# Performance work log

Hardware: AMD Instinct MI355X
Metric: run time of the kernel (lower is better)

## Reference

```python
import jax, jax.numpy as jnp
import numpy as np

N = 50000        # nodes
E = 600000       # edges
D = 128          # hidden dim
FID = 128        # fixed_input_dim (one-hot size)
RWSE = 16        # rwse_dim
G = 128          # num graphs
L = 4            # num GIN blocks
DEG = 1001       # degree embedding table (clamp to 1000)
GIN_EPS = 0.0
BN_EPS = 1e-5


def setup_inputs() -> dict:
    key = jax.random.key(0)
    ks = jax.random.split(key, 16)
    s = 0.05
    inp = {
        "feat_id": jax.random.randint(ks[0], (N,), 0, 100000),
        "edge_index": jax.random.randint(ks[1], (2, E), 0, N),
        "batch_idx": jnp.sort(jax.random.randint(ks[2], (N,), 0, G)),
        "rwse": jax.random.normal(ks[3], (N, RWSE), jnp.float32),
        "in_degrees": jax.random.randint(ks[4], (N,), 0, DEG),
        # parameters
        "value_W": jax.random.normal(ks[5], (FID, D), jnp.float32) * s,
        "value_b": jnp.zeros((D,), jnp.float32),
        "rwse_W": jax.random.normal(ks[6], (RWSE, D), jnp.float32) * s,
        "rwse_b": jnp.zeros((D,), jnp.float32),
        "deg_emb": jax.random.normal(ks[7], (DEG, D), jnp.float32) * s,
        "mlp_W1": jax.random.normal(ks[8], (L, D, D), jnp.float32) * s,
        "mlp_b1": jnp.zeros((L, D), jnp.float32),
        "mlp_W2": jax.random.normal(ks[9], (L, D, D), jnp.float32) * s,
        "mlp_b2": jnp.zeros((L, D), jnp.float32),
        "bn_gamma": 1.0 + jax.random.normal(ks[10], (L, D), jnp.float32) * s,
        "bn_beta": jax.random.normal(ks[11], (L, D), jnp.float32) * s,
        "bn_mean": jax.random.normal(ks[12], (L, D), jnp.float32) * s,
        "bn_var": 1.0 + jax.random.uniform(ks[13], (L, D), jnp.float32) * 0.1,
    }
    return inp


def reference(feat_id, edge_index, batch_idx, rwse, in_degrees,
              value_W, value_b, rwse_W, rwse_b, deg_emb,
              mlp_W1, mlp_b1, mlp_W2, mlp_b2,
              bn_gamma, bn_beta, bn_mean, bn_var):
    # one_hot(feat_id % FID) @ value_W  ==  row gather of value_W
    h_id = jnp.remainder(feat_id, FID)
    h_attr = value_W[h_id] + value_b                      # [N, D]
    h_attr = h_attr + rwse @ rwse_W + rwse_b              # rwse projection
    deg = jnp.clip(in_degrees, 0, DEG - 1)
    h = h_attr + deg_emb[deg]                             # [N, D]

    src, dst = edge_index[0], edge_index[1]
    for l in range(L):
        # GIN aggregation: sum of neighbor messages + (1+eps)*self
        agg = jax.ops.segment_sum(h[src], dst, num_segments=N)
        agg = agg + (1.0 + GIN_EPS) * h
        # MLP: Linear -> ReLU -> Linear
        m = jax.nn.relu(agg @ mlp_W1[l] + mlp_b1[l]) @ mlp_W2[l] + mlp_b2[l]
        # BatchNorm (inference stats) + ReLU
        inv = bn_gamma[l] * jax.lax.rsqrt(bn_var[l] + BN_EPS)
        h = jax.nn.relu((m - bn_mean[l]) * inv + bn_beta[l])

    # scatter-mean graph pooling
    pooled = jax.ops.segment_sum(h, batch_idx, num_segments=G)      # [G, D]
    count = jax.ops.segment_sum(jnp.ones((N, 1), h.dtype), batch_idx,
                                num_segments=G)                     # [G, 1]
    graph_feature = pooled / jnp.maximum(count, 1.0)
    return graph_feature, h
```

## Files before the change

### kernel.cpp

```cpp
#include <hip/hip_runtime.h>

#define N_NODES 50000
#define N_EDGES 600000
#define DIM 128
#define NGRAPH 128
#define NLAYER 4
#define BN_EPS 1e-5f
#define SCAN_BLK 1024
#define MROWS 64

#define EN_BLOCKS 3125
#define WT_BLOCKS 512
#define HB_BLOCKS 2344

using short8  = __attribute__((ext_vector_type(8))) short;
using float4v = __attribute__((ext_vector_type(4))) float;

__device__ __forceinline__ float bf2f(unsigned short u) {
    union { unsigned int i; float f; } c; c.i = ((unsigned int)u) << 16; return c.f;
}
__device__ __forceinline__ unsigned short f2bf(float f) {
    union { float f; unsigned int i; } c; c.f = f;
    unsigned int x = c.i;
    return (unsigned short)((x + 0x7fffu + ((x >> 16) & 1u)) >> 16);
}

__global__ void fused_pre_kernel(const int* __restrict__ feat_id,
                                 const float* __restrict__ rwse,
                                 const int* __restrict__ indeg,
                                 const float* __restrict__ value_W,
                                 const float* __restrict__ value_b,
                                 const float* __restrict__ rwse_W,
                                 const float* __restrict__ rwse_b,
                                 const float* __restrict__ deg_emb,
                                 unsigned short* __restrict__ hout,
                                 const float* __restrict__ W1,
                                 const float* __restrict__ W2,
                                 unsigned short* __restrict__ w1t,
                                 unsigned short* __restrict__ w2t,
                                 const int* __restrict__ dst,
                                 int* __restrict__ cnt)
{
    int b = blockIdx.x;
    if (b < EN_BLOCKS) {
        __shared__ float srw[16][16];
        __shared__ int   sfid[16], sdeg[16];
        const int t = threadIdx.x;
        const int base = b * 16;
        srw[t >> 4][t & 15] = rwse[(size_t)base * 16 + t];
        if (t < 16) sfid[t] = feat_id[base + t] & 127;
        else if (t < 32) {
            int dg = indeg[base + t - 16];
            sdeg[t - 16] = dg < 0 ? 0 : (dg > 1000 ? 1000 : dg);
        }
        const int d = t & 127, half = t >> 7;
        float wk[16];
#pragma unroll
        for (int k = 0; k < 16; ++k) wk[k] = rwse_W[k * DIM + d];
        float vb = value_b[d] + rwse_b[d];
        __syncthreads();
#pragma unroll
        for (int nn = 0; nn < 8; ++nn) {
            int nl = half * 8 + nn;
            int node = base + nl;
            float v = value_W[sfid[nl] * DIM + d] + vb + deg_emb[sdeg[nl] * DIM + d];
            float acc = 0.f;
#pragma unroll
            for (int k = 0; k < 16; ++k) acc += srw[nl][k] * wk[k];
            hout[(size_t)node * DIM + d] = f2bf(v + acc);
        }
    } else if (b < EN_BLOCKS + WT_BLOCKS) {
        int idx = (b - EN_BLOCKS) * 256 + threadIdx.x;
        int i = idx & (DIM * DIM - 1);
        int l = (idx >> 14) & 3;
        int is2 = idx >= NLAYER * DIM * DIM;
        int n = i >> 7, k = i & 127;
        const float* W = (is2 ? W2 : W1) + l * DIM * DIM;
        unsigned short v = f2bf(W[k * DIM + n]);
        (is2 ? w2t : w1t)[l * DIM * DIM + n * DIM + k] = v;
    } else {
        int e = (b - EN_BLOCKS - WT_BLOCKS) * 256 + threadIdx.x;
        if (e < N_EDGES) atomicAdd(&cnt[dst[e]], 1);
    }
}

__global__ void scanA_kernel(const int* __restrict__ cnt, int* __restrict__ rp, int* __restrict__ bsum) {
    __shared__ int sc[SCAN_BLK];
    int t = threadIdx.x, i = blockIdx.x * SCAN_BLK + t;
    int v = (i < N_NODES) ? cnt[i] : 0;
    sc[t] = v; __syncthreads();
    for (int off = 1; off < SCAN_BLK; off <<= 1) {
        int add = (t >= off) ? sc[t - off] : 0;
        __syncthreads();
        sc[t] += add;
        __syncthreads();
    }
    if (i < N_NODES) rp[i] = sc[t] - v;
    if (t == SCAN_BLK - 1) bsum[blockIdx.x] = sc[t];
}

__global__ void scan_fixup_kernel(int* __restrict__ rp, const int* __restrict__ bsum,
                                  int* __restrict__ cur, int nsb) {
    __shared__ int sbx[64];
    int t = threadIdx.x;
    if (t < 64) {
        int v = (t < nsb) ? bsum[t] : 0;
        int orig = v;
        for (int off = 1; off < 64; off <<= 1) {
            int y = __shfl_up(v, off, 64);
            if (t >= off) v += y;
        }
        sbx[t] = v - orig;
    }
    __syncthreads();
    int i = blockIdx.x * 256 + t;
    if (i < N_NODES) { int v = rp[i] + sbx[i >> 10]; rp[i] = v; cur[i] = v; }
    else if (i == N_NODES) rp[i] = N_EDGES;
}

__global__ void scatter_kernel(const int* __restrict__ src, const int* __restrict__ dst,
                               int* __restrict__ cur, int* __restrict__ esrc) {
    int e = blockIdx.x * blockDim.x + threadIdx.x;
    if (e < N_EDGES) {
        int pos = atomicAdd(&cur[dst[e]], 1);
        esrc[pos] = src[e];
    }
}

__global__ void __launch_bounds__(256) agg_kernel(const unsigned short* __restrict__ hin,
                                                  const int* __restrict__ rp,
                                                  const int* __restrict__ esrc,
                                                  unsigned short* __restrict__ aggout)
{
    int node = (blockIdx.x * blockDim.x + threadIdx.x) >> 6;
    node = __builtin_amdgcn_readfirstlane(node);
    if (node >= N_NODES) return;
    int lane = threadIdx.x & 63;
    int grp = lane >> 4, q = lane & 15;

    float a[8];
    if (grp == 0) {
        uint4 s = *(const uint4*)(hin + (size_t)node * DIM + q * 8);
        a[0] = bf2f((unsigned short)(s.x & 0xffff)); a[1] = bf2f((unsigned short)(s.x >> 16));
        a[2] = bf2f((unsigned short)(s.y & 0xffff)); a[3] = bf2f((unsigned short)(s.y >> 16));
        a[4] = bf2f((unsigned short)(s.z & 0xffff)); a[5] = bf2f((unsigned short)(s.z >> 16));
        a[6] = bf2f((unsigned short)(s.w & 0xffff)); a[7] = bf2f((unsigned short)(s.w >> 16));
    } else {
#pragma unroll
        for (int i = 0; i < 8; ++i) a[i] = 0.f;
    }

    const int e1 = rp[node + 1];
    int e = rp[node] + grp;
    bool p0 = e < e1, p1 = e + 4 < e1;
    int s0 = p0 ? esrc[e] : 0;
    int s1 = p1 ? esrc[e + 4] : 0;
    while (p0) {
        uint4 v0 = *(const uint4*)(hin + (size_t)s0 * DIM + q * 8);
        uint4 v1;
        if (p1) v1 = *(const uint4*)(hin + (size_t)s1 * DIM + q * 8);
        else v1 = (uint4){0u, 0u, 0u, 0u};
        e += 8;
        p0 = e < e1; p1 = e + 4 < e1;
        s0 = p0 ? esrc[e] : 0;
        s1 = p1 ? esrc[e + 4] : 0;
        a[0] += bf2f((unsigned short)(v0.x & 0xffff)) + bf2f((unsigned short)(v1.x & 0xffff));
        a[1] += bf2f((unsigned short)(v0.x >> 16))    + bf2f((unsigned short)(v1.x >> 16));
        a[2] += bf2f((unsigned short)(v0.y & 0xffff)) + bf2f((unsigned short)(v1.y & 0xffff));
        a[3] += bf2f((unsigned short)(v0.y >> 16))    + bf2f((unsigned short)(v1.y >> 16));
        a[4] += bf2f((unsigned short)(v0.z & 0xffff)) + bf2f((unsigned short)(v1.z & 0xffff));
        a[5] += bf2f((unsigned short)(v0.z >> 16))    + bf2f((unsigned short)(v1.z >> 16));
        a[6] += bf2f((unsigned short)(v0.w & 0xffff)) + bf2f((unsigned short)(v1.w & 0xffff));
        a[7] += bf2f((unsigned short)(v0.w >> 16))    + bf2f((unsigned short)(v1.w >> 16));
    }

#pragma unroll
    for (int i = 0; i < 8; ++i) {
        a[i] += __shfl_xor(a[i], 16, 64);
        a[i] += __shfl_xor(a[i], 32, 64);
    }

    if (grp == 0) {
        uint4 o;
        o.x = (unsigned int)f2bf(a[0]) | ((unsigned int)f2bf(a[1]) << 16);
        o.y = (unsigned int)f2bf(a[2]) | ((unsigned int)f2bf(a[3]) << 16);
        o.z = (unsigned int)f2bf(a[4]) | ((unsigned int)f2bf(a[5]) << 16);
        o.w = (unsigned int)f2bf(a[6]) | ((unsigned int)f2bf(a[7]) << 16);
        *(uint4*)(aggout + (size_t)node * DIM + q * 8) = o;
    }
}

__global__ void __launch_bounds__(256, 4) mlp_kernel(
    const unsigned short* __restrict__ aggin,
    const unsigned short* __restrict__ w1t,
    const unsigned short* __restrict__ w2t,
    const float* __restrict__ b1, const float* __restrict__ b2,
    const float* __restrict__ gam, const float* __restrict__ bet,
    const float* __restrict__ mean, const float* __restrict__ var,
    unsigned short* __restrict__ hout, float* __restrict__ fout, int last)
{
    __shared__ unsigned short sM[MROWS * DIM];
    const int tid = threadIdx.x;
    const int wave = tid >> 6, lane = tid & 63;
    const int fr = lane & 15, fg = lane >> 4;
    const int rowbase = blockIdx.x * MROWS;

    int arow = rowbase + wave * 16 + fr;
    if (arow >= N_NODES) arow = N_NODES - 1;
    const unsigned short* aptr = aggin + (size_t)arow * DIM + fg * 8;

    float4v acc[8];
#pragma unroll
    for (int n = 0; n < 8; ++n) acc[n] = (float4v){0.f, 0.f, 0.f, 0.f};

#pragma unroll
    for (int ks = 0; ks < 4; ++ks) {
        short8 a0 = *(const short8*)(aptr + ks * 32);
#pragma unroll
        for (int nb = 0; nb < 8; ++nb) {
            short8 b = *(const short8*)(w1t + (nb * 16 + fr) * DIM + ks * 32 + fg * 8);
            acc[nb] = __builtin_amdgcn_mfma_f32_16x16x32_bf16(a0, b, acc[nb], 0, 0, 0);
        }
    }

#pragma unroll
    for (int nb = 0; nb < 8; ++nb) {
        int col = nb * 16 + fr;
        float bias = b1[col];
#pragma unroll
        for (int r = 0; r < 4; ++r) {
            int row = wave * 16 + fg * 4 + r;
            float v = acc[nb][r] + bias;
            v = fmaxf(v, 0.f);
            int byte = row * 256 + col * 2; byte ^= (row & 7) << 4;
            *(unsigned short*)((char*)sM + byte) = f2bf(v);
        }
    }
    __syncthreads();

    float4v acc2[8];
#pragma unroll
    for (int n = 0; n < 8; ++n) acc2[n] = (float4v){0.f, 0.f, 0.f, 0.f};

#pragma unroll
    for (int ks = 0; ks < 4; ++ks) {
        int k0 = ks * 32 + fg * 8;
        short8 a0;
        { int row = wave * 16 + fr; int byte = row * 256 + k0 * 2; byte ^= (row & 7) << 4; a0 = *(const short8*)((char*)sM + byte); }
#pragma unroll
        for (int nb = 0; nb < 8; ++nb) {
            short8 b = *(const short8*)(w2t + (nb * 16 + fr) * DIM + k0);
            acc2[nb] = __builtin_amdgcn_mfma_f32_16x16x32_bf16(a0, b, acc2[nb], 0, 0, 0);
        }
    }

#pragma unroll
    for (int nb = 0; nb < 8; ++nb) {
        int col = nb * 16 + fr;
        float bias = b2[col];
        float iv = gam[col] * rsqrtf(var[col] + BN_EPS);
        float mn = mean[col], bt = bet[col];
#pragma unroll
        for (int r = 0; r < 4; ++r) {
            int row = wave * 16 + fg * 4 + r;
            int node = rowbase + row;
            if (node < N_NODES) {
                float v = acc2[nb][r] + bias;
                v = (v - mn) * iv + bt;
                v = fmaxf(v, 0.f);
                if (last) fout[(size_t)node * DIM + col] = v;
                else hout[(size_t)node * DIM + col] = f2bf(v);
            }
        }
    }
}

__global__ void __launch_bounds__(256) pool_partial_kernel(const float* __restrict__ h,
                                                           const int* __restrict__ batch,
                                                           float* __restrict__ partial)
{
    __shared__ float sums[256];
    __shared__ int sb[2];
    int g = blockIdx.x >> 3, split = blockIdx.x & 7;
    if (threadIdx.x < 2) {
        int target = g + threadIdx.x;
        int lo = 0, hi = N_NODES;
        while (lo < hi) { int mid = (lo + hi) >> 1; if (batch[mid] < target) lo = mid + 1; else hi = mid; }
        sb[threadIdx.x] = lo;
    }
    __syncthreads();
    int lo = sb[0], hi = sb[1];
    int d = threadIdx.x & 127, half = threadIdx.x >> 7;
    float acc = 0.f;
    for (int n = lo + split * 2 + half; n < hi; n += 16) acc += h[(size_t)n * DIM + d];
    sums[threadIdx.x] = acc;
    __syncthreads();
    if (threadIdx.x < 128)
        partial[blockIdx.x * DIM + threadIdx.x] = sums[threadIdx.x] + sums[threadIdx.x + 128];
}

__global__ void pool_comb_kernel(const float* __restrict__ partial,
                                 const int* __restrict__ batch,
                                 float* __restrict__ out)
{
    __shared__ int sb[2];
    int g = blockIdx.x, t = threadIdx.x;
    if (t < 2) {
        int target = g + t;
        int lo = 0, hi = N_NODES;
        while (lo < hi) { int mid = (lo + hi) >> 1; if (batch[mid] < target) lo = mid + 1; else hi = mid; }
        sb[t] = lo;
    }
    __syncthreads();
    float s = 0.f;
#pragma unroll
    for (int sp = 0; sp < 8; ++sp) s += partial[(g * 8 + sp) * DIM + t];
    float c = (float)(sb[1] - sb[0]);
    out[g * DIM + t] = s / fmaxf(c, 1.f);
}

extern "C" void kernel_launch(void* const* d_in, const int* in_sizes, int n_in,
                              void* d_out, int out_size, void* d_ws, size_t ws_size,
                              hipStream_t stream)
{
    const int*   feat_id = (const int*)d_in[0];
    const int*   eidx    = (const int*)d_in[1];
    const int*   batch   = (const int*)d_in[2];
    const float* rwse    = (const float*)d_in[3];
    const int*   indeg   = (const int*)d_in[4];
    const float* value_W = (const float*)d_in[5];
    const float* value_b = (const float*)d_in[6];
    const float* rwse_W  = (const float*)d_in[7];
    const float* rwse_b  = (const float*)d_in[8];
    const float* deg_emb = (const float*)d_in[9];
    const float* W1      = (const float*)d_in[10];
    const float* b1      = (const float*)d_in[11];
    const float* W2      = (const float*)d_in[12];
    const float* b2      = (const float*)d_in[13];
    const float* gam     = (const float*)d_in[14];
    const float* bet     = (const float*)d_in[15];
    const float* mean    = (const float*)d_in[16];
    const float* var     = (const float*)d_in[17];

    const int* srcv = eidx;
    const int* dstv = eidx + N_EDGES;

    char* p = (char*)d_ws;
    auto alloc = [&](size_t bytes) { char* r = p; p += (bytes + 255) & ~(size_t)255; return r; };
    unsigned short* hA   = (unsigned short*)alloc((size_t)N_NODES * DIM * 2);
    unsigned short* agg  = (unsigned short*)alloc((size_t)N_NODES * DIM * 2);
    int* cnt  = (int*)alloc((size_t)N_NODES * 4);
    int* rp   = (int*)alloc((size_t)(N_NODES + 1) * 4);
    int* cur  = (int*)alloc((size_t)N_NODES * 4);
    int* bsum = (int*)alloc(64 * 4);
    int* esrc = (int*)alloc((size_t)N_EDGES * 4);
    unsigned short* w1t = (unsigned short*)alloc((size_t)NLAYER * DIM * DIM * 2);
    unsigned short* w2t = (unsigned short*)alloc((size_t)NLAYER * DIM * DIM * 2);
    float* partial = (float*)alloc((size_t)NGRAPH * 8 * DIM * 4);

    float* out = (float*)d_out;
    float* hf  = out + NGRAPH * DIM;

    hipMemsetAsync(cnt, 0, (size_t)N_NODES * 4, stream);
    fused_pre_kernel<<<EN_BLOCKS + WT_BLOCKS + HB_BLOCKS, 256, 0, stream>>>(
        feat_id, rwse, indeg, value_W, value_b, rwse_W, rwse_b, deg_emb, hA,
        W1, W2, w1t, w2t, dstv, cnt);
    int nsb = (N_NODES + SCAN_BLK - 1) / SCAN_BLK;
    scanA_kernel<<<nsb, SCAN_BLK, 0, stream>>>(cnt, rp, bsum);
    scan_fixup_kernel<<<(N_NODES + 1 + 255) / 256, 256, 0, stream>>>(rp, bsum, cur, nsb);
    scatter_kernel<<<(N_EDGES + 255) / 256, 256, 0, stream>>>(srcv, dstv, cur, esrc);

    const int nrb = (N_NODES + MROWS - 1) / MROWS;
    for (int l = 0; l < NLAYER; ++l) {
        agg_kernel<<<(N_NODES * 64 + 255) / 256, 256, 0, stream>>>(hA, rp, esrc, agg);
        mlp_kernel<<<nrb, 256, 0, stream>>>(agg,
            w1t + l * DIM * DIM, w2t + l * DIM * DIM,
            b1 + l * DIM, b2 + l * DIM, gam + l * DIM, bet + l * DIM,
            mean + l * DIM, var + l * DIM,
            hA, hf, (l == NLAYER - 1) ? 1 : 0);
    }
    pool_partial_kernel<<<NGRAPH * 8, 256, 0, stream>>>(hf, batch, partial);
    pool_comb_kernel<<<NGRAPH, DIM, 0, stream>>>(partial, batch, out);
}
```

Baseline: 455.0 us.

## Shrink MLP blocks to one wave per 16 rows and simplify neighbor gather loop

The MLP kernel now runs one 64-thread wave per 16-row tile instead of four waves per 64 rows. It hoists all four A-operand k-slices into registers and loads the four B slices per output block together before issuing the MFMAs. Because 50000 divides by 16, the tail-row bounds checks are removed. The aggregation loop drops the two-edge unrolled gather in favor of one edge per iteration with the next source index prefetched, which reduces memory-level parallelism per lane. The smaller blocks give more scheduling granularity but shrink weight reuse across waves within a block.

```diff
diff --git a/kernel.cpp b/kernel.cpp
--- a/kernel.cpp
+++ b/kernel.cpp
@@ -7,7 +7,6 @@
 #define NLAYER 4
 #define BN_EPS 1e-5f
 #define SCAN_BLK 1024
-#define MROWS 64
 
 #define EN_BLOCKS 3125
 #define WT_BLOCKS 512
@@ -150,28 +149,19 @@
         for (int i = 0; i < 8; ++i) a[i] = 0.f;
     }
 
-    const int e1 = rp[node + 1];
+    int e1 = rp[node + 1];
     int e = rp[node] + grp;
-    bool p0 = e < e1, p1 = e + 4 < e1;
-    int s0 = p0 ? esrc[e] : 0;
-    int s1 = p1 ? esrc[e + 4] : 0;
-    while (p0) {
-        uint4 v0 = *(const uint4*)(hin + (size_t)s0 * DIM + q * 8);
-        uint4 v1;
-        if (p1) v1 = *(const uint4*)(hin + (size_t)s1 * DIM + q * 8);
-        else v1 = (uint4){0u, 0u, 0u, 0u};
-        e += 8;
-        p0 = e < e1; p1 = e + 4 < e1;
-        s0 = p0 ? esrc[e] : 0;
-        s1 = p1 ? esrc[e + 4] : 0;
-        a[0] += bf2f((unsigned short)(v0.x & 0xffff)) + bf2f((unsigned short)(v1.x & 0xffff));
-        a[1] += bf2f((unsigned short)(v0.x >> 16))    + bf2f((unsigned short)(v1.x >> 16));
-        a[2] += bf2f((unsigned short)(v0.y & 0xffff)) + bf2f((unsigned short)(v1.y & 0xffff));
-        a[3] += bf2f((unsigned short)(v0.y >> 16))    + bf2f((unsigned short)(v1.y >> 16));
-        a[4] += bf2f((unsigned short)(v0.z & 0xffff)) + bf2f((unsigned short)(v1.z & 0xffff));
-        a[5] += bf2f((unsigned short)(v0.z >> 16))    + bf2f((unsigned short)(v1.z >> 16));
-        a[6] += bf2f((unsigned short)(v0.w & 0xffff)) + bf2f((unsigned short)(v1.w & 0xffff));
-        a[7] += bf2f((unsigned short)(v0.w >> 16))    + bf2f((unsigned short)(v1.w >> 16));
+    int snext = (e < e1) ? esrc[e] : 0;
+    while (e < e1) {
+        int s = snext;
+        int en = e + 4;
+        snext = (en < e1) ? esrc[en] : 0;
+        uint4 v = *(const uint4*)(hin + (size_t)s * DIM + q * 8);
+        a[0] += bf2f((unsigned short)(v.x & 0xffff)); a[1] += bf2f((unsigned short)(v.x >> 16));
+        a[2] += bf2f((unsigned short)(v.y & 0xffff)); a[3] += bf2f((unsigned short)(v.y >> 16));
+        a[4] += bf2f((unsigned short)(v.z & 0xffff)); a[5] += bf2f((unsigned short)(v.z >> 16));
+        a[6] += bf2f((unsigned short)(v.w & 0xffff)); a[7] += bf2f((unsigned short)(v.w >> 16));
+        e = en;
     }
 
 #pragma unroll
@@ -190,7 +180,7 @@
     }
 }
 
-__global__ void __launch_bounds__(256, 4) mlp_kernel(
+__global__ void __launch_bounds__(64, 4) mlp_kernel(
     const unsigned short* __restrict__ aggin,
     const unsigned short* __restrict__ w1t,
     const unsigned short* __restrict__ w2t,
@@ -199,28 +189,33 @@
     const float* __restrict__ mean, const float* __restrict__ var,
     unsigned short* __restrict__ hout, float* __restrict__ fout, int last)
 {
-    __shared__ unsigned short sM[MROWS * DIM];
-    const int tid = threadIdx.x;
-    const int wave = tid >> 6, lane = tid & 63;
+    __shared__ unsigned short sM[16 * DIM];
+    const int lane = threadIdx.x;
     const int fr = lane & 15, fg = lane >> 4;
-    const int rowbase = blockIdx.x * MROWS;
-
-    int arow = rowbase + wave * 16 + fr;
-    if (arow >= N_NODES) arow = N_NODES - 1;
-    const unsigned short* aptr = aggin + (size_t)arow * DIM + fg * 8;
+    const int rowbase = blockIdx.x * 16;
+
+    const unsigned short* aptr = aggin + (size_t)(rowbase + fr) * DIM + fg * 8;
+    short8 a0 = *(const short8*)(aptr);
+    short8 a1 = *(const short8*)(aptr + 32);
+    short8 a2 = *(const short8*)(aptr + 64);
+    short8 a3 = *(const short8*)(aptr + 96);
 
     float4v acc[8];
 #pragma unroll
     for (int n = 0; n < 8; ++n) acc[n] = (float4v){0.f, 0.f, 0.f, 0.f};
 
-#pragma unroll
-    for (int ks = 0; ks < 4; ++ks) {
-        short8 a0 = *(const short8*)(aptr + ks * 32);
-#pragma unroll
-        for (int nb = 0; nb < 8; ++nb) {
-            short8 b = *(const short8*)(w1t + (nb * 16 + fr) * DIM + ks * 32 + fg * 8);
-            acc[nb] = __builtin_amdgcn_mfma_f32_16x16x32_bf16(a0, b, acc[nb], 0, 0, 0);
-        }
+    const unsigned short* bp1 = w1t + fr * DIM + fg * 8;
+#pragma unroll
+    for (int nb = 0; nb < 8; ++nb) {
+        const unsigned short* bb = bp1 + nb * 16 * DIM;
+        short8 b0 = *(const short8*)(bb);
+        short8 b1v = *(const short8*)(bb + 32);
+        short8 b2v = *(const short8*)(bb + 64);
+        short8 b3v = *(const short8*)(bb + 96);
+        acc[nb] = __builtin_amdgcn_mfma_f32_16x16x32_bf16(a0, b0, acc[nb], 0, 0, 0);
+        acc[nb] = __builtin_amdgcn_mfma_f32_16x16x32_bf16(a1, b1v, acc[nb], 0, 0, 0);
+        acc[nb] = __builtin_amdgcn_mfma_f32_16x16x32_bf16(a2, b2v, acc[nb], 0, 0, 0);
+        acc[nb] = __builtin_amdgcn_mfma_f32_16x16x32_bf16(a3, b3v, acc[nb], 0, 0, 0);
     }
 
 #pragma unroll
@@ -229,7 +224,7 @@
         float bias = b1[col];
 #pragma unroll
         for (int r = 0; r < 4; ++r) {
-            int row = wave * 16 + fg * 4 + r;
+            int row = fg * 4 + r;
             float v = acc[nb][r] + bias;
             v = fmaxf(v, 0.f);
             int byte = row * 256 + col * 2; byte ^= (row & 7) << 4;
@@ -238,20 +233,34 @@
     }
     __syncthreads();
 
+    short8 m0, m1, m2, m3;
+    {
+        int byte0 = fr * 256 + (fg * 8) * 2;       byte0 ^= (fr & 7) << 4;
+        int byte1 = fr * 256 + (32 + fg * 8) * 2;  byte1 ^= (fr & 7) << 4;
+        int byte2 = fr * 256 + (64 + fg * 8) * 2;  byte2 ^= (fr & 7) << 4;
+        int byte3 = fr * 256 + (96 + fg * 8) * 2;  byte3 ^= (fr & 7) << 4;
+        m0 = *(const short8*)((char*)sM + byte0);
+        m1 = *(const short8*)((char*)sM + byte1);
+        m2 = *(const short8*)((char*)sM + byte2);
+        m3 = *(const short8*)((char*)sM + byte3);
+    }
+
     float4v acc2[8];
 #pragma unroll
     for (int n = 0; n < 8; ++n) acc2[n] = (float4v){0.f, 0.f, 0.f, 0.f};
 
-#pragma unroll
-    for (int ks = 0; ks < 4; ++ks) {
-        int k0 = ks * 32 + fg * 8;
-        short8 a0;
-        { int row = wave * 16 + fr; int byte = row * 256 + k0 * 2; byte ^= (row & 7) << 4; a0 = *(const short8*)((char*)sM + byte); }
-#pragma unroll
-        for (int nb = 0; nb < 8; ++nb) {
-            short8 b = *(const short8*)(w2t + (nb * 16 + fr) * DIM + k0);
-            acc2[nb] = __builtin_amdgcn_mfma_f32_16x16x32_bf16(a0, b, acc2[nb], 0, 0, 0);
-        }
+    const unsigned short* bp2 = w2t + fr * DIM + fg * 8;
+#pragma unroll
+    for (int nb = 0; nb < 8; ++nb) {
+        const unsigned short* bb = bp2 + nb * 16 * DIM;
+        short8 b0 = *(const short8*)(bb);
+        short8 b1v = *(const short8*)(bb + 32);
+        short8 b2v = *(const short8*)(bb + 64);
+        short8 b3v = *(const short8*)(bb + 96);
+        acc2[nb] = __builtin_amdgcn_mfma_f32_16x16x32_bf16(m0, b0, acc2[nb], 0, 0, 0);
+        acc2[nb] = __builtin_amdgcn_mfma_f32_16x16x32_bf16(m1, b1v, acc2[nb], 0, 0, 0);
+        acc2[nb] = __builtin_amdgcn_mfma_f32_16x16x32_bf16(m2, b2v, acc2[nb], 0, 0, 0);
+        acc2[nb] = __builtin_amdgcn_mfma_f32_16x16x32_bf16(m3, b3v, acc2[nb], 0, 0, 0);
     }
 
 #pragma unroll
@@ -262,15 +271,12 @@
         float mn = mean[col], bt = bet[col];
 #pragma unroll
         for (int r = 0; r < 4; ++r) {
-            int row = wave * 16 + fg * 4 + r;
-            int node = rowbase + row;
-            if (node < N_NODES) {
-                float v = acc2[nb][r] + bias;
-                v = (v - mn) * iv + bt;
-                v = fmaxf(v, 0.f);
-                if (last) fout[(size_t)node * DIM + col] = v;
-                else hout[(size_t)node * DIM + col] = f2bf(v);
-            }
+            int node = rowbase + fg * 4 + r;
+            float v = acc2[nb][r] + bias;
+            v = (v - mn) * iv + bt;
+            v = fmaxf(v, 0.f);
+            if (last) fout[(size_t)node * DIM + col] = v;
+            else hout[(size_t)node * DIM + col] = f2bf(v);
         }
     }
 }
@@ -370,10 +376,10 @@
     scan_fixup_kernel<<<(N_NODES + 1 + 255) / 256, 256, 0, stream>>>(rp, bsum, cur, nsb);
     scatter_kernel<<<(N_EDGES + 255) / 256, 256, 0, stream>>>(srcv, dstv, cur, esrc);
 
-    const int nrb = (N_NODES + MROWS - 1) / MROWS;
+    const int nrb = N_NODES / 16;
     for (int l = 0; l < NLAYER; ++l) {
         agg_kernel<<<(N_NODES * 64 + 255) / 256, 256, 0, stream>>>(hA, rp, esrc, agg);
-        mlp_kernel<<<nrb, 256, 0, stream>>>(agg,
+        mlp_kernel<<<nrb, 64, 0, stream>>>(agg,
             w1t + l * DIM * DIM, w2t + l * DIM * DIM,
             b1 + l * DIM, b2 + l * DIM, gam + l * DIM, bet + l * DIM,
             mean + l * DIM, var + l * DIM,
```

New measurement: 435.3 us. 1.05x faster.
